# Performance work log

Hardware: AMD Instinct MI355X
Metric: run time of the kernel (lower is better)

## Reference

```python
import jax, jax.numpy as jnp
import numpy as np

K = 9   # kernel_size (neighbors)
D = 1   # dilation


def setup_inputs() -> dict:
    key = jax.random.key(0)
    k1, k2 = jax.random.split(key)
    B, C, N, OUT = 8, 64, 4096, 128
    x = jax.random.normal(k1, (B, C, N), dtype=jnp.float32)
    W = jax.random.normal(k2, (OUT, 2 * C), dtype=jnp.float32) * 0.05
    b = jnp.zeros((OUT,), dtype=jnp.float32)
    return {"x": x, "W": W, "b": b}


def dilated_knn(x, k, d):
    # x: [B, C, N] -> nn_idx: [B, N, k] (indices of k nearest neighbors, dilated)
    x = jax.lax.stop_gradient(x)  # original detaches x for graph construction
    x2 = jnp.sum(x * x, axis=1)                      # [B, N]
    inner = jnp.einsum('bcn,bcm->bnm', x, x)         # [B, N, N]
    neg_dist = 2.0 * inner - x2[:, :, None] - x2[:, None, :]  # -||xi-xj||^2
    _, idx = jax.lax.top_k(neg_dist, k * d)          # [B, N, k*d]
    return idx[..., ::d]                             # dilated selection -> [B, N, k]


def reference(x, W, b):
    # x: [B, C, N]
    nn_idx = dilated_knn(x, K, D)                    # [B, N, k]
    # gather neighbor features: x_j[b, c, n, kk] = x[b, c, nn_idx[b, n, kk]]
    x_j = jax.vmap(lambda xb, ib: xb[:, ib])(x, nn_idx)  # [B, C, N, k]
    # max-relative: max_k (x_j - x_i)
    x_max = jnp.max(x_j - x[:, :, :, None], axis=-1)     # [B, C, N]
    h = jnp.concatenate([x, x_max], axis=1)              # [B, 2C, N]
    # 1x1 conv + bias + ReLU
    out = jnp.einsum('oc,bcn->bon', W, h) + b[None, :, None]
    return jax.nn.relu(out)
```

## Files before the change

kernel.cpp:

```cpp
#include <hip/hip_runtime.h>
#include <float.h>

#define B_   8
#define C_   64
#define N_   4096
#define OUT_ 128
#define KNN  9
#define CAP  64
#define TAU_A 2.15f

typedef __attribute__((ext_vector_type(8))) short short8;
typedef __attribute__((ext_vector_type(4))) float f32x4;

__device__ inline unsigned short f2bf(float f) {
    unsigned u = __float_as_uint(f);
    unsigned r = (u + 0x7fffu + ((u >> 16) & 1u)) >> 16;
    return (unsigned short)r;
}
__device__ inline float bf2f(unsigned short s) {
    return __uint_as_float(((unsigned)s) << 16);
}


__global__ void k_wt(const float* __restrict__ W, unsigned short* __restrict__ wfrag) {
    int mt = blockIdx.x, kc = threadIdx.x >> 6, L = threadIdx.x & 63;
    int o  = mt * 16 + (L & 15);
    int c0 = kc * 32 + ((L >> 4) * 8);
    const float* src = W + (size_t)o * 128 + c0;
    float4 v0 = *(const float4*)src, v1 = *(const float4*)(src + 4);
    float vs[8] = {v0.x, v0.y, v0.z, v0.w, v1.x, v1.y, v1.z, v1.w};
    short8 hi, lo;
#pragma unroll
    for (int j = 0; j < 8; ++j) {
        unsigned short hb = f2bf(vs[j]);
        float hf = bf2f(hb);
        lo[j] = (short)f2bf(vs[j] - hf);
        hi[j] = (short)hb;
    }
    size_t cb = (size_t)(mt * 4 + kc) * 2 * 512;
    *(short8*)(wfrag + cb + L * 8)       = hi;
    *(short8*)(wfrag + cb + 512 + L * 8) = lo;
}

__global__ void k_transpose(const float* __restrict__ x, float* __restrict__ xT,
                            float* __restrict__ x2, unsigned short* __restrict__ xfrag) {
    __shared__ float t[C_][65];
    int b  = blockIdx.x & 7;
    int n0 = (blockIdx.x >> 3) * 64;
    int tid = threadIdx.x;
    for (int i = 0; i < 16; ++i) {
        int e = i * 256 + tid;
        int c = e >> 6, nn = e & 63;
        t[c][nn] = x[((size_t)b * C_ + c) * N_ + n0 + nn];
    }
    __syncthreads();
    for (int i = 0; i < 16; ++i) {
        int e = i * 256 + tid;
        int nn = e >> 6, c = e & 63;
        xT[((size_t)b * N_ + n0 + nn) * C_ + c] = t[c][nn];
    }
    int q = tid >> 6, L = tid & 63;
    int mloc = q * 16 + (L & 15);
    int k8 = (L >> 4) * 8;
    size_t cb = (size_t)(b * 256 + (n0 >> 4) + q) * 2 * 512;
#pragma unroll
    for (int h = 0; h < 2; ++h) {
        short8 hi;
#pragma unroll
        for (int j = 0; j < 8; ++j)
            hi[j] = (short)f2bf(t[h * 32 + k8 + j][mloc]);
        *(short8*)(xfrag + cb + h * 512 + L * 8) = hi;
    }
    if (tid < 64) {
        float s = 0.f;
        for (int c = 0; c < C_; ++c) { float v = t[c][tid]; s += v * v; }
        x2[(size_t)b * N_ + n0 + tid] = s;
    }
}

#define APPEND(KEY, TAU, LN, MIDX)                                      \
    if ((KEY) > (TAU)) {                                                \
        unsigned u = __float_as_uint(KEY);                              \
        u = (u & 0x80000000u) ? ~u : (u | 0x80000000u);                 \
        unsigned pk = (u & 0xFFFFF000u) | (unsigned)(MIDX);             \
        int sl = atomicAdd(&cnt_s[LN], 1);                              \
        if (sl < CAP) buf_s[LN][sl] = pk;                               \
    }

#define TILE_COMPUTE(AH0, AH1, X2V, MBASE)                              \
    _Pragma("unroll")                                                   \
    for (int q = 0; q < 4; ++q) {                                       \
        f32x4 acc = {0.f, 0.f, 0.f, 0.f};                               \
        acc = __builtin_amdgcn_mfma_f32_16x16x32_bf16(AH0, Bh[q][0], acc, 0, 0, 0); \
        acc = __builtin_amdgcn_mfma_f32_16x16x32_bf16(AH1, Bh[q][1], acc, 0, 0, 0); \
        float k0 = fmaf(2.f, acc[0], -(X2V)[0]);                        \
        float k1 = fmaf(2.f, acc[1], -(X2V)[1]);                        \
        float k2 = fmaf(2.f, acc[2], -(X2V)[2]);                        \
        float k3 = fmaf(2.f, acc[3], -(X2V)[3]);                        \
        float kmax = fmaxf(fmaxf(k0, k1), fmaxf(k2, k3));               \
        if (kmax > tau[q]) {                                            \
            int ln = q * 16 + (lane & 15);                              \
            APPEND(k0, tau[q], ln, (MBASE) + 0)                         \
            APPEND(k1, tau[q], ln, (MBASE) + 1)                         \
            APPEND(k2, tau[q], ln, (MBASE) + 2)                         \
            APPEND(k3, tau[q], ln, (MBASE) + 3)                         \
        }                                                               \
    }

__global__ __launch_bounds__(512, 4) void k_topk_mf(const unsigned short* __restrict__ xfrag,
                                                    const float* __restrict__ x2,
                                                    unsigned* __restrict__ cand24,
                                                    int* __restrict__ cnt2) {
    __shared__ int cnt_s[64];
    __shared__ unsigned buf_s[64][CAP];
    int b    = blockIdx.x & 7;
    int mh   = (blockIdx.x >> 3) & 1;
    int ng   = blockIdx.x >> 4;
    int wave = threadIdx.x >> 6, lane = threadIdx.x & 63;
    if (threadIdx.x < 64) cnt_s[threadIdx.x] = 0;

    const short8* fr = (const short8*)xfrag;

    short8 Bh[4][2];
#pragma unroll
    for (int q = 0; q < 4; ++q)
#pragma unroll
        for (int h = 0; h < 2; ++h) {
            int ch = ((b * 256 + ng * 4 + q) * 2 + h);
            Bh[q][h] = fr[(size_t)ch * 64 + lane];
        }

    float tau[4];
#pragma unroll
    for (int q = 0; q < 4; ++q) {
        float x2n = x2[b * N_ + ng * 64 + q * 16 + (lane & 15)];
        tau[q] = TAU_A * sqrtf(fmaf(4.f, x2n, 128.f)) - 64.f;
    }

    int mt0 = mh * 128 + wave * 16;
    const short8* pA = fr + (size_t)(b * 256 + mt0) * 2 * 64 + lane;
    const f32x4*  px2 = (const f32x4*)(x2 + b * N_ + mt0 * 16 + (lane >> 4) * 4);

    short8 Ph0 = pA[0], Ph1 = pA[64];
    f32x4  xp  = px2[0];
    pA += 128; px2 += 4;
    short8 Qh0 = pA[0], Qh1 = pA[64];
    f32x4  xq  = px2[0];

    __syncthreads();

    for (int i = 0; i < 16; ++i) {
        pA += 128; px2 += 4;
        short8 Rh0 = pA[0], Rh1 = pA[64];
        f32x4  xr  = px2[0];

        int mbase = (mt0 + i) * 16 + (lane >> 4) * 4;
        TILE_COMPUTE(Ph0, Ph1, xp, mbase)

        Ph0 = Qh0; Ph1 = Qh1; xp = xq;
        Qh0 = Rh0; Qh1 = Rh1; xq = xr;
    }

    __syncthreads();
    if (threadIdx.x < 64) {
        int r = threadIdx.x;
        int c = cnt_s[r];
        size_t grow = (size_t)b * N_ + ng * 64 + r;
        cnt2[grow * 2 + mh] = c;
        int cc = min(c, CAP);
        unsigned best[12];
#pragma unroll
        for (int j = 0; j < 12; ++j) best[j] = 0u;
        for (int s = 0; s < cc; ++s) {
            unsigned v = buf_s[r][s];
            if (v > best[0]) {
                best[0] = v;
#pragma unroll
                for (int j = 0; j < 11; ++j) {
                    bool sw = best[j] > best[j + 1];
                    unsigned t = best[j];
                    best[j]     = sw ? best[j + 1] : best[j];
                    best[j + 1] = sw ? t : best[j + 1];
                }
            }
        }
#pragma unroll
        for (int j = 0; j < 12; ++j)
            cand24[grow * 24 + mh * 12 + j] = best[11 - j];
    }
}

__global__ __launch_bounds__(256) void k_refine(const float* __restrict__ xT,
                                                const unsigned* __restrict__ cand24,
                                                const int* __restrict__ cnt2,
                                                int* __restrict__ idx9) {
    __shared__ double kk[4][2][24];
    __shared__ int    ki[4][2][24];
    int wave = threadIdx.x >> 6, lane = threadIdx.x & 63;
    int half = lane >> 5, hl = lane & 31;
    int b = blockIdx.x & 7;
    int row = b * N_ + (blockIdx.x >> 3) * 8 + wave * 2 + half;
    int c0 = cnt2[(size_t)row * 2 + 0];
    int c1 = cnt2[(size_t)row * 2 + 1];
    bool ok = (c0 + c1 >= KNN) && (c0 <= CAP) && (c1 <= CAP);
    int c0c = min(c0, 12), c1c = min(c1, 12);

    double mykey = -1e300; int myidx = 0x7fffffff;
    bool valid = ok && (hl < 24) && ((hl < 12) ? (hl < c0c) : ((hl - 12) < c1c));
    if (valid) {
        int m = (int)(cand24[(size_t)row * 24 + hl] & 0xFFFu);
        const float* xi = xT + (size_t)row * C_;
        const float* xm = xT + (((size_t)b << 12) + m) * C_;
        double d0 = 0.0, d1 = 0.0, s0 = 0.0, s1 = 0.0;
#pragma unroll
        for (int c4 = 0; c4 < 16; c4 += 2) {
            float4 a0 = *(const float4*)(xi + c4 * 4);
            float4 a1 = *(const float4*)(xi + c4 * 4 + 4);
            float4 v0 = *(const float4*)(xm + c4 * 4);
            float4 v1 = *(const float4*)(xm + c4 * 4 + 4);
            d0 = fma((double)a0.x, (double)v0.x, d0);  s0 = fma((double)v0.x, (double)v0.x, s0);
            d0 = fma((double)a0.y, (double)v0.y, d0);  s0 = fma((double)v0.y, (double)v0.y, s0);
            d0 = fma((double)a0.z, (double)v0.z, d0);  s0 = fma((double)v0.z, (double)v0.z, s0);
            d0 = fma((double)a0.w, (double)v0.w, d0);  s0 = fma((double)v0.w, (double)v0.w, s0);
            d1 = fma((double)a1.x, (double)v1.x, d1);  s1 = fma((double)v1.x, (double)v1.x, s1);
            d1 = fma((double)a1.y, (double)v1.y, d1);  s1 = fma((double)v1.y, (double)v1.y, s1);
            d1 = fma((double)a1.z, (double)v1.z, d1);  s1 = fma((double)v1.z, (double)v1.z, s1);
            d1 = fma((double)a1.w, (double)v1.w, d1);  s1 = fma((double)v1.w, (double)v1.w, s1);
        }
        mykey = 2.0 * (d0 + d1) - (s0 + s1);
        myidx = m;
    }
    if (hl < 24) { kk[wave][half][hl] = mykey; ki[wave][half][hl] = myidx; }
    if (valid) {
        int r = 0;
#pragma unroll
        for (int k = 0; k < 24; ++k) {
            double ok2 = kk[wave][half][k]; int oi = ki[wave][half][k];
            r += (ok2 > mykey || (ok2 == mykey && oi < myidx)) ? 1 : 0;
        }
        if (r < KNN) idx9[(size_t)row * KNN + r] = myidx;
    }
}

__global__ void k_fallback(const float* __restrict__ xT, const int* __restrict__ cnt2,
                           int* __restrict__ idx9) {
    int wave = threadIdx.x >> 6, lane = threadIdx.x & 63;
    int row = blockIdx.x * 4 + wave;
    int c0 = cnt2[(size_t)row * 2 + 0];
    int c1 = cnt2[(size_t)row * 2 + 1];
    if ((c0 + c1 >= KNN) && (c0 <= CAP) && (c1 <= CAP)) return;
    int b = row >> 12;
    const float* xi = xT + (size_t)row * C_;
    float4 xr[16];
#pragma unroll
    for (int c4 = 0; c4 < 16; ++c4) xr[c4] = *(const float4*)(xi + c4 * 4);
    double sk[9]; int si[9];
#pragma unroll
    for (int j = 0; j < 9; ++j) { sk[j] = -1e300; si[j] = 0x7fffffff; }
    for (int mb = 0; mb < N_; mb += 64) {
        int m = mb + lane;
        const float* xm = xT + (((size_t)b << 12) + m) * C_;
        double d0 = 0.0, d1 = 0.0, s0 = 0.0, s1 = 0.0;
#pragma unroll
        for (int c4 = 0; c4 < 16; c4 += 2) {
            float4 v = *(const float4*)(xm + c4 * 4);
            float4 w = *(const float4*)(xm + c4 * 4 + 4);
            float4 a = xr[c4], bb = xr[c4 + 1];
            d0 = fma((double)a.x, (double)v.x, d0);  s0 = fma((double)v.x, (double)v.x, s0);
            d0 = fma((double)a.y, (double)v.y, d0);  s0 = fma((double)v.y, (double)v.y, s0);
            d0 = fma((double)a.z, (double)v.z, d0);  s0 = fma((double)v.z, (double)v.z, s0);
            d0 = fma((double)a.w, (double)v.w, d0);  s0 = fma((double)v.w, (double)v.w, s0);
            d1 = fma((double)bb.x, (double)w.x, d1); s1 = fma((double)w.x, (double)w.x, s1);
            d1 = fma((double)bb.y, (double)w.y, d1); s1 = fma((double)w.y, (double)w.y, s1);
            d1 = fma((double)bb.z, (double)w.z, d1); s1 = fma((double)w.z, (double)w.z, s1);
            d1 = fma((double)bb.w, (double)w.w, d1); s1 = fma((double)w.w, (double)w.w, s1);
        }
        double key = 2.0 * (d0 + d1) - (s0 + s1);
        if (key > sk[0] || (key == sk[0] && m < si[0])) {
            sk[0] = key; si[0] = m;
#pragma unroll
            for (int j = 0; j < 8; ++j) {
                bool sw = (sk[j] > sk[j + 1]) || (sk[j] == sk[j + 1] && si[j] < si[j + 1]);
                double tk = sk[j]; int ti = si[j];
                sk[j]     = sw ? sk[j + 1] : sk[j];
                si[j]     = sw ? si[j + 1] : si[j];
                sk[j + 1] = sw ? tk : sk[j + 1];
                si[j + 1] = sw ? ti : si[j + 1];
            }
        }
    }
    for (int r = 0; r < KNN; ++r) {
        double k = sk[8]; int ix = si[8];
#pragma unroll
        for (int o = 32; o; o >>= 1) {
            double ok = __shfl_xor(k, o); int oi = __shfl_xor(ix, o);
            bool take = (ok > k) || (ok == k && oi < ix);
            k = take ? ok : k; ix = take ? oi : ix;
        }
        if (lane == 0) idx9[(size_t)row * KNN + r] = ix;
        if (si[8] == ix) {
#pragma unroll
            for (int j = 8; j > 0; --j) { sk[j] = sk[j - 1]; si[j] = si[j - 1]; }
            sk[0] = -1e300; si[0] = 0x7fffffff;
        }
    }
}

__global__ __launch_bounds__(256, 2) void k_gemm(const float* __restrict__ xT,
                                                 const int* __restrict__ idx9,
                                                 const unsigned short* __restrict__ wfrag,
                                                 const float* __restrict__ bias,
                                                 float* __restrict__ out) {
    __shared__ float h[128][65];
    int b  = blockIdx.x & 7;
    int n0 = (blockIdx.x >> 3) * 64;
    int wave = threadIdx.x >> 6, lane = threadIdx.x & 63;

    const short8* fw = (const short8*)wfrag;
    short8 Wh[2][4], Wl[2][4];
#pragma unroll
    for (int t = 0; t < 2; ++t)
#pragma unroll
        for (int kc = 0; kc < 4; ++kc) {
            size_t cb = (size_t)((wave * 2 + t) * 4 + kc) * 2 * 64;
            Wh[t][kc] = fw[cb + lane];
            Wl[t][kc] = fw[cb + 64 + lane];
        }

    for (int r = 0; r < 16; ++r) {
        int nn = wave * 16 + r;
        size_t row = (size_t)b * N_ + n0 + nn;
        const int* id = idx9 + row * KNN;
        float m = -FLT_MAX;
#pragma unroll
        for (int k = 0; k < KNN; ++k) {
            int j = id[k];
            m = fmaxf(m, xT[(((size_t)b << 12) + j) * C_ + lane]);
        }
        float xic = xT[row * C_ + lane];
        h[lane][nn]      = xic;
        h[64 + lane][nn] = m - xic;
    }
    __syncthreads();

    f32x4 acc[2][4];
#pragma unroll
    for (int t = 0; t < 2; ++t)
#pragma unroll
        for (int nt = 0; nt < 4; ++nt) acc[t][nt] = (f32x4){0.f, 0.f, 0.f, 0.f};

    int cb0 = (lane >> 4) * 8;
    int nl  = lane & 15;
#pragma unroll
    for (int kc = 0; kc < 4; ++kc) {
#pragma unroll
        for (int nt = 0; nt < 4; ++nt) {
            short8 bh, bl;
#pragma unroll
            for (int j = 0; j < 8; ++j) {
                float v = h[kc * 32 + cb0 + j][nt * 16 + nl];
                unsigned short hb = f2bf(v);
                bl[j] = (short)f2bf(v - bf2f(hb));
                bh[j] = (short)hb;
            }
#pragma unroll
            for (int t = 0; t < 2; ++t) {
                acc[t][nt] = __builtin_amdgcn_mfma_f32_16x16x32_bf16(Wh[t][kc], bh, acc[t][nt], 0, 0, 0);
                acc[t][nt] = __builtin_amdgcn_mfma_f32_16x16x32_bf16(Wl[t][kc], bh, acc[t][nt], 0, 0, 0);
                acc[t][nt] = __builtin_amdgcn_mfma_f32_16x16x32_bf16(Wh[t][kc], bl, acc[t][nt], 0, 0, 0);
            }
        }
    }
    __syncthreads();

    f32x4 bs[2];
#pragma unroll
    for (int t = 0; t < 2; ++t)
        bs[t] = *(const f32x4*)(bias + wave * 32 + t * 16 + (lane >> 4) * 4);
#pragma unroll
    for (int t = 0; t < 2; ++t)
#pragma unroll
        for (int nt = 0; nt < 4; ++nt)
#pragma unroll
            for (int j = 0; j < 4; ++j) {
                float v = acc[t][nt][j] + bs[t][j];
                h[wave * 32 + t * 16 + (lane >> 4) * 4 + j][nt * 16 + nl] = fmaxf(v, 0.f);
            }
    __syncthreads();

#pragma unroll
    for (int rr = 0; rr < 32; ++rr) {
        int o = wave * 32 + rr;
        out[((size_t)b * OUT_ + o) * N_ + n0 + lane] = h[o][lane];
    }
}

extern "C" void kernel_launch(void* const* d_in, const int* in_sizes, int n_in,
                              void* d_out, int out_size, void* d_ws, size_t ws_size,
                              hipStream_t stream) {
    const float* x    = (const float*)d_in[0];
    const float* W    = (const float*)d_in[1];
    const float* bias = (const float*)d_in[2];
    float* out = (float*)d_out;
    char* ws = (char*)d_ws;

    float*          xT     = (float*)(ws);
    unsigned short* xfrag  = (unsigned short*)(ws + 8388608);
    int*            idx9   = (int*)(ws + 8388608);
    float*          x2     = (float*)(ws + 16777216);
    unsigned short* wfrag  = (unsigned short*)(ws + 16908288);
    unsigned*       cand24 = (unsigned*)(ws + 16973824);
    int*            cnt2   = (int*)(ws + 20119552);

    k_wt       <<<dim3(8),    dim3(256), 0, stream>>>(W, wfrag);
    k_transpose<<<dim3(512),  dim3(256), 0, stream>>>(x, xT, x2, xfrag);
    k_topk_mf  <<<dim3(1024), dim3(512), 0, stream>>>(xfrag, x2, cand24, cnt2);
    k_refine   <<<dim3(4096), dim3(256), 0, stream>>>(xT, cand24, cnt2, idx9);
    k_fallback <<<dim3(8192), dim3(256), 0, stream>>>(xT, cnt2, idx9);
    k_gemm     <<<dim3(512),  dim3(256), 0, stream>>>(xT, idx9, wfrag, bias, out);
}
```

Measured before the change: 120.9 us.

## Split top-k candidate search into four column quarters per row block

The MFMA top-k kernel now splits the candidate column range into four quarters with 256-thread blocks instead of two halves with 512-thread blocks. This doubles the grid to raise occupancy and parallelism. Each row then keeps up to 48 candidates, and the refine kernel handles one row per wave, ranking 48 instead of 24 in double precision. The trade-off is more candidate traffic, more refine work, and a larger per-block selection overhead.

```diff
diff --git a/kernel.cpp b/kernel.cpp
--- a/kernel.cpp
+++ b/kernel.cpp
@@ -107,15 +107,15 @@
         }                                                               \
     }
 
-__global__ __launch_bounds__(512, 4) void k_topk_mf(const unsigned short* __restrict__ xfrag,
+__global__ __launch_bounds__(256, 8) void k_topk_mf(const unsigned short* __restrict__ xfrag,
                                                     const float* __restrict__ x2,
-                                                    unsigned* __restrict__ cand24,
-                                                    int* __restrict__ cnt2) {
+                                                    unsigned* __restrict__ cand48,
+                                                    int* __restrict__ cnt4) {
     __shared__ int cnt_s[64];
     __shared__ unsigned buf_s[64][CAP];
     int b    = blockIdx.x & 7;
-    int mh   = (blockIdx.x >> 3) & 1;
-    int ng   = blockIdx.x >> 4;
+    int mq   = (blockIdx.x >> 3) & 3;
+    int ng   = blockIdx.x >> 5;
     int wave = threadIdx.x >> 6, lane = threadIdx.x & 63;
     if (threadIdx.x < 64) cnt_s[threadIdx.x] = 0;
 
@@ -137,7 +137,7 @@
         tau[q] = TAU_A * sqrtf(fmaf(4.f, x2n, 128.f)) - 64.f;
     }
 
-    int mt0 = mh * 128 + wave * 16;
+    int mt0 = mq * 64 + wave * 16;
     const short8* pA = fr + (size_t)(b * 256 + mt0) * 2 * 64 + lane;
     const f32x4*  px2 = (const f32x4*)(x2 + b * N_ + mt0 * 16 + (lane >> 4) * 4);
 
@@ -166,7 +166,7 @@
         int r = threadIdx.x;
         int c = cnt_s[r];
         size_t grow = (size_t)b * N_ + ng * 64 + r;
-        cnt2[grow * 2 + mh] = c;
+        cnt4[grow * 4 + mq] = c;
         int cc = min(c, CAP);
         unsigned best[12];
 #pragma unroll
@@ -186,29 +186,32 @@
         }
 #pragma unroll
         for (int j = 0; j < 12; ++j)
-            cand24[grow * 24 + mh * 12 + j] = best[11 - j];
+            cand48[grow * 48 + mq * 12 + j] = best[11 - j];
     }
 }
 
 __global__ __launch_bounds__(256) void k_refine(const float* __restrict__ xT,
-                                                const unsigned* __restrict__ cand24,
-                                                const int* __restrict__ cnt2,
+                                                const unsigned* __restrict__ cand48,
+                                                const int* __restrict__ cnt4,
                                                 int* __restrict__ idx9) {
-    __shared__ double kk[4][2][24];
-    __shared__ int    ki[4][2][24];
+    __shared__ double kk[4][48];
+    __shared__ int    ki[4][48];
     int wave = threadIdx.x >> 6, lane = threadIdx.x & 63;
-    int half = lane >> 5, hl = lane & 31;
     int b = blockIdx.x & 7;
-    int row = b * N_ + (blockIdx.x >> 3) * 8 + wave * 2 + half;
-    int c0 = cnt2[(size_t)row * 2 + 0];
-    int c1 = cnt2[(size_t)row * 2 + 1];
-    bool ok = (c0 + c1 >= KNN) && (c0 <= CAP) && (c1 <= CAP);
-    int c0c = min(c0, 12), c1c = min(c1, 12);
+    int row = b * N_ + (blockIdx.x >> 3) * 4 + wave;
+    int c0 = cnt4[(size_t)row * 4 + 0];
+    int c1 = cnt4[(size_t)row * 4 + 1];
+    int c2 = cnt4[(size_t)row * 4 + 2];
+    int c3 = cnt4[(size_t)row * 4 + 3];
+    int cmax = max(max(c0, c1), max(c2, c3));
+    bool ok = (c0 + c1 + c2 + c3 >= KNN) && (cmax <= CAP);
+    int qq = lane / 12, slot = lane - qq * 12;
+    int cq = (qq == 0) ? c0 : (qq == 1) ? c1 : (qq == 2) ? c2 : c3;
 
     double mykey = -1e300; int myidx = 0x7fffffff;
-    bool valid = ok && (hl < 24) && ((hl < 12) ? (hl < c0c) : ((hl - 12) < c1c));
+    bool valid = ok && (lane < 48) && (slot < min(cq, 12));
     if (valid) {
-        int m = (int)(cand24[(size_t)row * 24 + hl] & 0xFFFu);
+        int m = (int)(cand48[(size_t)row * 48 + lane] & 0xFFFu);
         const float* xi = xT + (size_t)row * C_;
         const float* xm = xT + (((size_t)b << 12) + m) * C_;
         double d0 = 0.0, d1 = 0.0, s0 = 0.0, s1 = 0.0;
@@ -230,25 +233,28 @@
         mykey = 2.0 * (d0 + d1) - (s0 + s1);
         myidx = m;
     }
-    if (hl < 24) { kk[wave][half][hl] = mykey; ki[wave][half][hl] = myidx; }
+    if (lane < 48) { kk[wave][lane] = mykey; ki[wave][lane] = myidx; }
     if (valid) {
         int r = 0;
 #pragma unroll
-        for (int k = 0; k < 24; ++k) {
-            double ok2 = kk[wave][half][k]; int oi = ki[wave][half][k];
+        for (int k = 0; k < 48; ++k) {
+            double ok2 = kk[wave][k]; int oi = ki[wave][k];
             r += (ok2 > mykey || (ok2 == mykey && oi < myidx)) ? 1 : 0;
         }
         if (r < KNN) idx9[(size_t)row * KNN + r] = myidx;
     }
 }
 
-__global__ void k_fallback(const float* __restrict__ xT, const int* __restrict__ cnt2,
+__global__ void k_fallback(const float* __restrict__ xT, const int* __restrict__ cnt4,
                            int* __restrict__ idx9) {
     int wave = threadIdx.x >> 6, lane = threadIdx.x & 63;
     int row = blockIdx.x * 4 + wave;
-    int c0 = cnt2[(size_t)row * 2 + 0];
-    int c1 = cnt2[(size_t)row * 2 + 1];
-    if ((c0 + c1 >= KNN) && (c0 <= CAP) && (c1 <= CAP)) return;
+    int c0 = cnt4[(size_t)row * 4 + 0];
+    int c1 = cnt4[(size_t)row * 4 + 1];
+    int c2 = cnt4[(size_t)row * 4 + 2];
+    int c3 = cnt4[(size_t)row * 4 + 3];
+    int cmax = max(max(c0, c1), max(c2, c3));
+    if ((c0 + c1 + c2 + c3 >= KNN) && (cmax <= CAP)) return;
     int b = row >> 12;
     const float* xi = xT + (size_t)row * C_;
     float4 xr[16];
@@ -409,13 +415,13 @@
     int*            idx9   = (int*)(ws + 8388608);
     float*          x2     = (float*)(ws + 16777216);
     unsigned short* wfrag  = (unsigned short*)(ws + 16908288);
-    unsigned*       cand24 = (unsigned*)(ws + 16973824);
-    int*            cnt2   = (int*)(ws + 20119552);
+    unsigned*       cand48 = (unsigned*)(ws + 16973824);
+    int*            cnt4   = (int*)(ws + 23265280);
 
     k_wt       <<<dim3(8),    dim3(256), 0, stream>>>(W, wfrag);
     k_transpose<<<dim3(512),  dim3(256), 0, stream>>>(x, xT, x2, xfrag);
-    k_topk_mf  <<<dim3(1024), dim3(512), 0, stream>>>(xfrag, x2, cand24, cnt2);
-    k_refine   <<<dim3(4096), dim3(256), 0, stream>>>(xT, cand24, cnt2, idx9);
-    k_fallback <<<dim3(8192), dim3(256), 0, stream>>>(xT, cnt2, idx9);
+    k_topk_mf  <<<dim3(2048), dim3(256), 0, stream>>>(xfrag, x2, cand48, cnt4);
+    k_refine   <<<dim3(8192), dim3(256), 0, stream>>>(xT, cand48, cnt4, idx9);
+    k_fallback <<<dim3(8192), dim3(256), 0, stream>>>(xT, cnt4, idx9);
     k_gemm     <<<dim3(512),  dim3(256), 0, stream>>>(xT, idx9, wfrag, bias, out);
 }
```

New measurement: 313.2 us. 159% more time.
